# Optimization experiments

Hardware: AMD Instinct MI355X
Metric: run time of the kernel (lower is better)

Reference implementation:

```python
import jax, jax.numpy as jnp
import numpy as np

I_DIM = 50000
D_DIM = 128
N_EDGES = 800000
N_NODES = I_DIM + 1


def setup_inputs() -> dict:
    key = jax.random.key(0)
    k1, k2, k3, k4 = jax.random.split(key, 4)
    # edge[:,0] must be sorted for the original bincount+repeat normalization to be valid
    src = jnp.sort(jax.random.randint(k1, (N_EDGES,), 0, N_NODES))
    dst = jax.random.randint(k2, (N_EDGES,), 0, N_NODES)
    edge = jnp.stack([src, dst], axis=1).astype(jnp.int64)
    # GlorotNormal-style init for the embedding table and dense layers
    emb_mat = jax.random.normal(k3, (N_NODES, D_DIM), dtype=jnp.float32) * np.sqrt(2.0 / (N_NODES + D_DIM))
    kA, kB = jax.random.split(k4)
    W_scale = jax.random.normal(kA, (D_DIM, D_DIM), dtype=jnp.float32) * np.sqrt(2.0 / (2 * D_DIM))
    b_scale = jnp.zeros((D_DIM,), dtype=jnp.float32)
    W_att = jax.random.normal(kB, (2 * D_DIM, 1), dtype=jnp.float32) * np.sqrt(2.0 / (2 * D_DIM + 1))
    b_att = jnp.zeros((1,), dtype=jnp.float32)
    return {"edge": edge, "emb_mat": emb_mat, "W_scale": W_scale,
            "b_scale": b_scale, "W_att": W_att, "b_att": b_att}


def reference(edge, emb_mat, W_scale, b_scale, W_att, b_att):
    E = edge.shape[0]
    src = edge[:, 0]
    dst = edge[:, 1]
    # gather both endpoints, project: [E, 2, d]
    edge_emb = jnp.einsum('epd,df->epf', emb_mat[edge], W_scale) + b_scale
    edge_emb = edge_emb.reshape(E, -1)                       # [E, 2d]
    att = edge_emb @ W_att + b_att                           # [E, 1]
    att = jnp.where(att >= 0, att, 0.2 * att)                # LeakyReLU(0.2)
    att = jnp.squeeze(att, axis=-1)                          # [E]
    scores = jnp.exp(att - 1.0)
    score_sum = jax.ops.segment_sum(scores, src, num_segments=N_NODES)
    score_norm = scores / score_sum[src]                     # segment softmax
    item_scaled = emb_mat @ W_scale + b_scale                # [N, d]
    msgs = score_norm[:, None] * item_scaled[dst]            # [E, d]
    agg = jax.ops.segment_sum(msgs, src, num_segments=N_NODES)
    return jax.nn.sigmoid(agg)                               # [N, d]
```

## Files before the change

### kernel.cpp

```cpp
#include <hip/hip_runtime.h>
#include <math.h>

#define NN 50001
#define DD 128
#define NE 800000

typedef __attribute__((ext_vector_type(8))) short short8;
typedef __attribute__((ext_vector_type(4))) float floatx4;

__device__ __forceinline__ unsigned short f2bf(float f) {
    unsigned u = __builtin_bit_cast(unsigned, f);
    u += 0x7fffu + ((u >> 16) & 1u);
    return (unsigned short)(u >> 16);
}
__device__ __forceinline__ float bflo(unsigned u) {
    return __builtin_bit_cast(float, u << 16);
}
__device__ __forceinline__ float bfhi(unsigned u) {
    return __builtin_bit_cast(float, u & 0xffff0000u);
}

__global__ void k_wt(const float* __restrict__ W, unsigned short* __restrict__ WT) {
    int idx = blockIdx.x * blockDim.x + threadIdx.x;
    if (idx < DD * DD) {
        int k = idx >> 7, j = idx & 127;
        WT[j * DD + k] = f2bf(W[idx]);
    }
}

__global__ void k_rowptr(const int* __restrict__ edge, int* __restrict__ row_ptr) {
    int e = blockIdx.x * blockDim.x + threadIdx.x;
    if (e >= NE) return;
    int s = edge[2 * e];
    if (e == 0) {
        for (int n = 0; n <= s; n++) row_ptr[n] = 0;
    } else {
        int p = edge[2 * (e - 1)];
        for (int n = p + 1; n <= s; n++) row_ptr[n] = e;
    }
    if (e == NE - 1) {
        for (int n = s + 1; n <= NN; n++) row_ptr[n] = NE;
    }
}

__global__ void __launch_bounds__(256) k_gemm(const float* __restrict__ emb,
        const unsigned short* __restrict__ WT, const float* __restrict__ b_scale,
        const float* __restrict__ W_att, unsigned short* __restrict__ item,
        float* __restrict__ a_src, float* __restrict__ a_dst) {
    int wave = blockIdx.x * 4 + (threadIdx.x >> 6);
    int lane = threadIdx.x & 63;
    int base = wave * 16;
    if (base >= NN) return;
    int m = lane & 15, q = lane >> 4;

    int row = base + m; if (row >= NN) row = NN - 1;
    const float* ap = emb + (long)row * DD + q * 8;
    short8 a[4];
    #pragma unroll
    for (int ks = 0; ks < 4; ks++) {
        const float* p = ap + ks * 32;
        #pragma unroll
        for (int j = 0; j < 8; j++) a[ks][j] = (short)f2bf(p[j]);
    }

    float p_src[4] = {0.f, 0.f, 0.f, 0.f};
    float p_dst[4] = {0.f, 0.f, 0.f, 0.f};

    #pragma unroll
    for (int ft = 0; ft < 8; ft++) {
        int col = ft * 16 + m;
        floatx4 acc = {0.f, 0.f, 0.f, 0.f};
        #pragma unroll
        for (int ks = 0; ks < 4; ks++) {
            short8 b = *(const short8*)(WT + col * DD + ks * 32 + q * 8);
            acc = __builtin_amdgcn_mfma_f32_16x16x32_bf16(a[ks], b, acc, 0, 0, 0);
        }
        float bs = b_scale[col];
        float wsrc = W_att[col], wdst = W_att[DD + col];
        #pragma unroll
        for (int r = 0; r < 4; r++) {
            float v = acc[r] + bs;
            int gr = base + q * 4 + r;
            if (gr < NN) item[(long)gr * DD + col] = f2bf(v);
            p_src[r] += v * wsrc;
            p_dst[r] += v * wdst;
        }
    }
    #pragma unroll
    for (int off = 1; off <= 8; off <<= 1) {
        #pragma unroll
        for (int r = 0; r < 4; r++) {
            p_src[r] += __shfl_xor(p_src[r], off, 64);
            p_dst[r] += __shfl_xor(p_dst[r], off, 64);
        }
    }
    if (m == 0) {
        #pragma unroll
        for (int r = 0; r < 4; r++) {
            int gr = base + q * 4 + r;
            if (gr < NN) { a_src[gr] = p_src[r]; a_dst[gr] = p_dst[r]; }
        }
    }
}

__global__ void __launch_bounds__(256) k_agg(const int* __restrict__ edge,
        const int* __restrict__ row_ptr, const unsigned short* __restrict__ item,
        const float* __restrict__ a_src, const float* __restrict__ a_dst,
        const float* __restrict__ b_att, float* __restrict__ out) {
    int n = blockIdx.x * 4 + (threadIdx.x >> 6);
    int lane = threadIdx.x & 63;
    if (n >= NN) return;
    int g = lane >> 4, t = lane & 15;

    int start = row_ptr[n], end = row_ptr[n + 1];

    if (end > start) {
        float asrc = a_src[n] + b_att[0];
        float acc[8] = {0.f, 0.f, 0.f, 0.f, 0.f, 0.f, 0.f, 0.f};
        float ssum = 0.f;
        for (int b = start; b < end; b += 64) {
            int cnt = min(64, end - b);
            int d = 0; float s = 0.f;
            if (lane < cnt) {
                int e = b + lane;
                d = edge[2 * e + 1];
                float att = asrc + a_dst[d];
                att = att >= 0.f ? att : 0.2f * att;
                s = __expf(att - 1.f);
            }
            ssum += s;
            int ngroups = (cnt + 3) >> 2;
            for (int i = 0; i < ngroups; i++) {
                int j = 4 * i + g;
                float sj = __shfl(s, j);
                int   dj = __shfl(d, j);
                const uint4 u = *(const uint4*)(item + (long)dj * DD + t * 8);
                acc[0] += sj * bflo(u.x); acc[1] += sj * bfhi(u.x);
                acc[2] += sj * bflo(u.y); acc[3] += sj * bfhi(u.y);
                acc[4] += sj * bflo(u.z); acc[5] += sj * bfhi(u.z);
                acc[6] += sj * bflo(u.w); acc[7] += sj * bfhi(u.w);
            }
        }
        #pragma unroll
        for (int off = 16; off <= 32; off <<= 1) {
            #pragma unroll
            for (int k = 0; k < 8; k++) acc[k] += __shfl_xor(acc[k], off, 64);
        }
        #pragma unroll
        for (int off = 1; off < 64; off <<= 1) ssum += __shfl_xor(ssum, off, 64);

        if (g == 0) {
            float inv = 1.f / ssum;
            float4 o0, o1;
            o0.x = 1.f / (1.f + __expf(-acc[0] * inv));
            o0.y = 1.f / (1.f + __expf(-acc[1] * inv));
            o0.z = 1.f / (1.f + __expf(-acc[2] * inv));
            o0.w = 1.f / (1.f + __expf(-acc[3] * inv));
            o1.x = 1.f / (1.f + __expf(-acc[4] * inv));
            o1.y = 1.f / (1.f + __expf(-acc[5] * inv));
            o1.z = 1.f / (1.f + __expf(-acc[6] * inv));
            o1.w = 1.f / (1.f + __expf(-acc[7] * inv));
            float* op = out + (long)n * DD + t * 8;
            *(float4*)op = o0;
            *(float4*)(op + 4) = o1;
        }
    } else {
        if (g == 0) {
            float4 h = make_float4(0.5f, 0.5f, 0.5f, 0.5f);
            float* op = out + (long)n * DD + t * 8;
            *(float4*)op = h;
            *(float4*)(op + 4) = h;
        }
    }
}

extern "C" void kernel_launch(void* const* d_in, const int* in_sizes, int n_in,
                              void* d_out, int out_size, void* d_ws, size_t ws_size,
                              hipStream_t stream) {
    const int*   edge    = (const int*)d_in[0];
    const float* emb     = (const float*)d_in[1];
    const float* W_scale = (const float*)d_in[2];
    const float* b_scale = (const float*)d_in[3];
    const float* W_att   = (const float*)d_in[4];
    const float* b_att   = (const float*)d_in[5];
    float* out = (float*)d_out;

    char* ws = (char*)d_ws;
    unsigned short* WT      = (unsigned short*)(ws);
    int*            row_ptr = (int*)(ws + 32768);
    float*          a_src   = (float*)(ws + 32768 + 200832);
    float*          a_dst   = (float*)(ws + 32768 + 200832 + 200192);
    unsigned short* item    = (unsigned short*)(ws + 32768 + 200832 + 2 * 200192);

    int node_blocks = (NN + 3) / 4;
    int tile_blocks = ((NN + 15) / 16 + 3) / 4;
    int edge_blocks = (NE + 255) / 256;

    k_wt    <<<64,          256, 0, stream>>>(W_scale, WT);
    k_rowptr<<<edge_blocks, 256, 0, stream>>>(edge, row_ptr);
    k_gemm  <<<tile_blocks, 256, 0, stream>>>(emb, WT, b_scale, W_att, item, a_src, a_dst);
    k_agg   <<<node_blocks, 256, 0, stream>>>(edge, row_ptr, item, a_src, a_dst, b_att, out);
}
```

Baseline: 148.9 us.

## Precompute per-edge scores in a separate kernel and simplify aggregation loop

Merges the weight-transpose and row-pointer kernels into one launch. Adds a per-edge kernel that computes each softmax score and packs it with the destination index, so the aggregation kernel drops its shuffle-broadcast loop and streams (dst, score) pairs directly. The GEMM loads inputs as float4, and the sigmoid epilogue is split across two lane groups. This adds an extra launch plus a 6.4MB intermediate write and read in exchange for a simpler, more latency-tolerant gather loop.

```diff
diff --git a/kernel.cpp b/kernel.cpp
--- a/kernel.cpp
+++ b/kernel.cpp
@@ -20,26 +20,26 @@
     return __builtin_bit_cast(float, u & 0xffff0000u);
 }
 
-__global__ void k_wt(const float* __restrict__ W, unsigned short* __restrict__ WT) {
-    int idx = blockIdx.x * blockDim.x + threadIdx.x;
-    if (idx < DD * DD) {
+__global__ void k_prep(const float* __restrict__ W, unsigned short* __restrict__ WT,
+                       const int* __restrict__ edge, int* __restrict__ row_ptr) {
+    int b = blockIdx.x;
+    if (b < 64) {
+        int idx = b * 256 + threadIdx.x;
         int k = idx >> 7, j = idx & 127;
         WT[j * DD + k] = f2bf(W[idx]);
-    }
-}
-
-__global__ void k_rowptr(const int* __restrict__ edge, int* __restrict__ row_ptr) {
-    int e = blockIdx.x * blockDim.x + threadIdx.x;
-    if (e >= NE) return;
-    int s = edge[2 * e];
-    if (e == 0) {
-        for (int n = 0; n <= s; n++) row_ptr[n] = 0;
     } else {
-        int p = edge[2 * (e - 1)];
-        for (int n = p + 1; n <= s; n++) row_ptr[n] = e;
-    }
-    if (e == NE - 1) {
-        for (int n = s + 1; n <= NN; n++) row_ptr[n] = NE;
+        int e = (b - 64) * 256 + threadIdx.x;
+        if (e >= NE) return;
+        int s = edge[2 * e];
+        if (e == 0) {
+            for (int n = 0; n <= s; n++) row_ptr[n] = 0;
+        } else {
+            int p = edge[2 * (e - 1)];
+            for (int n = p + 1; n <= s; n++) row_ptr[n] = e;
+        }
+        if (e == NE - 1) {
+            for (int n = s + 1; n <= NN; n++) row_ptr[n] = NE;
+        }
     }
 }
 
@@ -58,9 +58,12 @@
     short8 a[4];
     #pragma unroll
     for (int ks = 0; ks < 4; ks++) {
-        const float* p = ap + ks * 32;
-        #pragma unroll
-        for (int j = 0; j < 8; j++) a[ks][j] = (short)f2bf(p[j]);
+        float4 f0 = *(const float4*)(ap + ks * 32);
+        float4 f1 = *(const float4*)(ap + ks * 32 + 4);
+        a[ks][0] = (short)f2bf(f0.x); a[ks][1] = (short)f2bf(f0.y);
+        a[ks][2] = (short)f2bf(f0.z); a[ks][3] = (short)f2bf(f0.w);
+        a[ks][4] = (short)f2bf(f1.x); a[ks][5] = (short)f2bf(f1.y);
+        a[ks][6] = (short)f2bf(f1.z); a[ks][7] = (short)f2bf(f1.w);
     }
 
     float p_src[4] = {0.f, 0.f, 0.f, 0.f};
@@ -103,74 +106,69 @@
     }
 }
 
-__global__ void __launch_bounds__(256) k_agg(const int* __restrict__ edge,
-        const int* __restrict__ row_ptr, const unsigned short* __restrict__ item,
+__global__ void __launch_bounds__(256) k_score(const int* __restrict__ edge,
         const float* __restrict__ a_src, const float* __restrict__ a_dst,
-        const float* __restrict__ b_att, float* __restrict__ out) {
+        const float* __restrict__ b_att, uint2* __restrict__ sd) {
+    int e = blockIdx.x * 256 + threadIdx.x;
+    if (e >= NE) return;
+    int2 ed = ((const int2*)edge)[e];
+    float att = a_src[ed.x] + a_dst[ed.y] + b_att[0];
+    att = att >= 0.f ? att : 0.2f * att;
+    float s = __expf(att - 1.f);
+    sd[e] = make_uint2((unsigned)ed.y, __builtin_bit_cast(unsigned, s));
+}
+
+__global__ void __launch_bounds__(256) k_agg(const int* __restrict__ row_ptr,
+        const uint2* __restrict__ sd, const unsigned short* __restrict__ item,
+        float* __restrict__ out) {
     int n = blockIdx.x * 4 + (threadIdx.x >> 6);
     int lane = threadIdx.x & 63;
     if (n >= NN) return;
     int g = lane >> 4, t = lane & 15;
 
-    int start = row_ptr[n], end = row_ptr[n + 1];
-
-    if (end > start) {
-        float asrc = a_src[n] + b_att[0];
+    int start = row_ptr[n];
+    int len = row_ptr[n + 1] - start;
+
+    if (len > 0) {
         float acc[8] = {0.f, 0.f, 0.f, 0.f, 0.f, 0.f, 0.f, 0.f};
         float ssum = 0.f;
-        for (int b = start; b < end; b += 64) {
-            int cnt = min(64, end - b);
-            int d = 0; float s = 0.f;
-            if (lane < cnt) {
-                int e = b + lane;
-                d = edge[2 * e + 1];
-                float att = asrc + a_dst[d];
-                att = att >= 0.f ? att : 0.2f * att;
-                s = __expf(att - 1.f);
-            }
-            ssum += s;
-            int ngroups = (cnt + 3) >> 2;
-            for (int i = 0; i < ngroups; i++) {
-                int j = 4 * i + g;
-                float sj = __shfl(s, j);
-                int   dj = __shfl(d, j);
-                const uint4 u = *(const uint4*)(item + (long)dj * DD + t * 8);
-                acc[0] += sj * bflo(u.x); acc[1] += sj * bfhi(u.x);
-                acc[2] += sj * bflo(u.y); acc[3] += sj * bfhi(u.y);
-                acc[4] += sj * bflo(u.z); acc[5] += sj * bfhi(u.z);
-                acc[6] += sj * bflo(u.w); acc[7] += sj * bfhi(u.w);
-            }
+        const uint2* sp = sd + start;
+        #pragma unroll 2
+        for (int j = g; j < len; j += 4) {
+            uint2 p = sp[j];
+            float sj = __builtin_bit_cast(float, p.y);
+            ssum += sj;
+            const uint4 u = *(const uint4*)(item + (long)p.x * DD + t * 8);
+            acc[0] += sj * bflo(u.x); acc[1] += sj * bfhi(u.x);
+            acc[2] += sj * bflo(u.y); acc[3] += sj * bfhi(u.y);
+            acc[4] += sj * bflo(u.z); acc[5] += sj * bfhi(u.z);
+            acc[6] += sj * bflo(u.w); acc[7] += sj * bfhi(u.w);
         }
         #pragma unroll
         for (int off = 16; off <= 32; off <<= 1) {
             #pragma unroll
             for (int k = 0; k < 8; k++) acc[k] += __shfl_xor(acc[k], off, 64);
-        }
-        #pragma unroll
-        for (int off = 1; off < 64; off <<= 1) ssum += __shfl_xor(ssum, off, 64);
-
+            ssum += __shfl_xor(ssum, off, 64);
+        }
+        float inv = 1.f / ssum;
+        float4 o;
         if (g == 0) {
-            float inv = 1.f / ssum;
-            float4 o0, o1;
-            o0.x = 1.f / (1.f + __expf(-acc[0] * inv));
-            o0.y = 1.f / (1.f + __expf(-acc[1] * inv));
-            o0.z = 1.f / (1.f + __expf(-acc[2] * inv));
-            o0.w = 1.f / (1.f + __expf(-acc[3] * inv));
-            o1.x = 1.f / (1.f + __expf(-acc[4] * inv));
-            o1.y = 1.f / (1.f + __expf(-acc[5] * inv));
-            o1.z = 1.f / (1.f + __expf(-acc[6] * inv));
-            o1.w = 1.f / (1.f + __expf(-acc[7] * inv));
-            float* op = out + (long)n * DD + t * 8;
-            *(float4*)op = o0;
-            *(float4*)(op + 4) = o1;
+            o.x = 1.f / (1.f + __expf(-acc[0] * inv));
+            o.y = 1.f / (1.f + __expf(-acc[1] * inv));
+            o.z = 1.f / (1.f + __expf(-acc[2] * inv));
+            o.w = 1.f / (1.f + __expf(-acc[3] * inv));
+            *(float4*)(out + (long)n * DD + t * 8) = o;
+        } else if (g == 1) {
+            o.x = 1.f / (1.f + __expf(-acc[4] * inv));
+            o.y = 1.f / (1.f + __expf(-acc[5] * inv));
+            o.z = 1.f / (1.f + __expf(-acc[6] * inv));
+            o.w = 1.f / (1.f + __expf(-acc[7] * inv));
+            *(float4*)(out + (long)n * DD + t * 8 + 4) = o;
         }
     } else {
-        if (g == 0) {
-            float4 h = make_float4(0.5f, 0.5f, 0.5f, 0.5f);
-            float* op = out + (long)n * DD + t * 8;
-            *(float4*)op = h;
-            *(float4*)(op + 4) = h;
-        }
+        float4 h = make_float4(0.5f, 0.5f, 0.5f, 0.5f);
+        if (g == 0)      *(float4*)(out + (long)n * DD + t * 8) = h;
+        else if (g == 1) *(float4*)(out + (long)n * DD + t * 8 + 4) = h;
     }
 }
 
@@ -188,16 +186,17 @@
     char* ws = (char*)d_ws;
     unsigned short* WT      = (unsigned short*)(ws);
     int*            row_ptr = (int*)(ws + 32768);
-    float*          a_src   = (float*)(ws + 32768 + 200832);
-    float*          a_dst   = (float*)(ws + 32768 + 200832 + 200192);
-    unsigned short* item    = (unsigned short*)(ws + 32768 + 200832 + 2 * 200192);
+    float*          a_src   = (float*)(ws + 233600);
+    float*          a_dst   = (float*)(ws + 433792);
+    unsigned short* item    = (unsigned short*)(ws + 633984);
+    uint2*          sd      = (uint2*)(ws + 13434240);
 
     int node_blocks = (NN + 3) / 4;
     int tile_blocks = ((NN + 15) / 16 + 3) / 4;
     int edge_blocks = (NE + 255) / 256;
 
-    k_wt    <<<64,          256, 0, stream>>>(W_scale, WT);
-    k_rowptr<<<edge_blocks, 256, 0, stream>>>(edge, row_ptr);
-    k_gemm  <<<tile_blocks, 256, 0, stream>>>(emb, WT, b_scale, W_att, item, a_src, a_dst);
-    k_agg   <<<node_blocks, 256, 0, stream>>>(edge, row_ptr, item, a_src, a_dst, b_att, out);
-}
+    k_prep <<<64 + edge_blocks, 256, 0, stream>>>(W_scale, WT, edge, row_ptr);
+    k_gemm <<<tile_blocks,      256, 0, stream>>>(emb, WT, b_scale, W_att, item, a_src, a_dst);
+    k_score<<<edge_blocks,      256, 0, stream>>>(edge, a_src, a_dst, b_att, sd);
+    k_agg  <<<node_blocks,      256, 0, stream>>>(row_ptr, sd, item, out);
+}
```

After: 146.3 us. About the same (-1.8%).
